# Performance work log

Measured on AMD Instinct MI355X. Metric: run time of the kernel, lower is better.

The kernel has to match this reference:

```python
import jax, jax.numpy as jnp
import numpy as np

T, IN, BATCH = 512, 512, 256
HID, WID = 1024, 512


def setup_inputs() -> dict:
    key = jax.random.key(0)
    k_x, k_wh, k_bh, k_wy, k_by, k_h0 = jax.random.split(key, 6)
    s_h = 1.0 / np.sqrt(HID + IN)  # stabilise sigmoid pre-activations
    s_y = 1.0 / np.sqrt(HID)
    return {
        "xs": jax.random.normal(k_x, (T, IN, BATCH), dtype=jnp.float32),
        "W_h": jax.random.normal(k_wh, (HID, HID + IN), dtype=jnp.float32) * s_h,
        "b_h": jax.random.normal(k_bh, (HID, 1), dtype=jnp.float32) * 0.1,
        "W_y": jax.random.normal(k_wy, (WID, HID), dtype=jnp.float32) * s_y,
        "b_y": jax.random.normal(k_by, (WID, 1), dtype=jnp.float32) * 0.1,
        "h0": jax.random.normal(k_h0, (HID, 1), dtype=jnp.float32),
    }


def reference(xs, W_h, b_h, W_y, b_y, h0):
    # xs: [T, input_size, batch]; returns ys: [T, width, batch]
    batch = xs.shape[2]
    h_init = jnp.tile(h0, (1, batch))  # [HID, batch]

    def step(h, x):
        z = jnp.concatenate([h, x], axis=0)          # [HID+IN, batch]
        h_new = jax.nn.sigmoid(W_h @ z + b_h)        # [HID, batch]
        y = jax.nn.sigmoid(W_y @ h_new + b_y)        # [WID, batch]
        return h_new, y

    _, ys = jax.lax.scan(step, h_init, xs)
    return ys
```

## Files before the change

kernel.cpp:

```cpp
#include <hip/hip_runtime.h>
#include <hip/hip_bf16.h>

#define T_STEPS 512
#define INP     512
#define NB      256
#define HID     1024
#define WID     512
#define KZ      1536
#define ZSZ     (NB * KZ)
#define ZR      6

typedef short          bf16x8   __attribute__((ext_vector_type(8)));
typedef float          f32x4    __attribute__((ext_vector_type(4)));
typedef float          f32x2    __attribute__((ext_vector_type(2)));
typedef unsigned short ushort8  __attribute__((ext_vector_type(8)));
typedef unsigned short ushort2v __attribute__((ext_vector_type(2)));
typedef unsigned short ushort4v __attribute__((ext_vector_type(4)));
typedef unsigned       uint4v   __attribute__((ext_vector_type(4)));
typedef unsigned long long u64;

__device__ __forceinline__ unsigned short f2bf(float x) {
  __hip_bfloat16 h = __float2bfloat16(x);
  return __builtin_bit_cast(unsigned short, h);
}
__device__ __forceinline__ float sigm(float x) { return 1.0f / (1.0f + __expf(-x)); }

#define ZLOAD_FAST(dst, p) \
  asm volatile("global_load_dwordx4 %0, %1, off sc0" : "=v"(dst) : "v"(p))
#define ZLOAD_SLOW(dst, p) \
  asm volatile("global_load_dwordx4 %0, %1, off sc0 sc1" : "=v"(dst) : "v"(p))
#define ZWAITN(n) do { \
  asm volatile("s_waitcnt vmcnt(" #n ")" ::: "memory"); \
  __builtin_amdgcn_sched_barrier(0); \
} while (0)

template <bool FAST>
__device__ __forceinline__ void zst4(unsigned short* p, ushort2v v) {
  if constexpr (FAST) *(unsigned*)p = __builtin_bit_cast(unsigned, v);
  else __hip_atomic_store((unsigned*)p, __builtin_bit_cast(unsigned, v),
                          __ATOMIC_RELAXED, __HIP_MEMORY_SCOPE_AGENT);
}
template <bool FAST>
__device__ __forceinline__ void zst8(unsigned short* p, ushort4v v) {
  if constexpr (FAST) *(u64*)p = __builtin_bit_cast(u64, v);
  else __hip_atomic_store((u64*)p, __builtin_bit_cast(u64, v),
                          __ATOMIC_RELAXED, __HIP_MEMORY_SCOPE_AGENT);
}

__device__ __forceinline__ void poll1(unsigned* p, unsigned tgt) {
  while (__hip_atomic_load(p, __ATOMIC_RELAXED, __HIP_MEMORY_SCOPE_AGENT) < tgt)
    __builtin_amdgcn_s_sleep(1);
}
__device__ __forceinline__ void pollh(unsigned* bar, unsigned ht, unsigned xt, unsigned yt) {
  uint4v v;
  for (;;) {
    asm volatile("global_load_dwordx4 %0, %1, off sc0 sc1\n\ts_waitcnt vmcnt(0)"
                 : "=v"(v) : "v"(bar) : "memory");
    if (v.x >= ht && v.y >= xt && v.z >= yt) return;
    __builtin_amdgcn_s_sleep(1);
  }
}
__device__ __forceinline__ void arrive(unsigned* ctr) {
  asm volatile("s_waitcnt vmcnt(0)" ::: "memory");
  __syncthreads();
  if (threadIdx.x == 0)
    __hip_atomic_fetch_add(ctr, 1u, __ATOMIC_RELAXED, __HIP_MEMORY_SCOPE_AGENT);
}

__global__ void elman_setup(const float* __restrict__ h0, const float* __restrict__ xs,
                            unsigned short* __restrict__ zT, unsigned* __restrict__ bars) {
  const int b = blockIdx.x;
  if (b == 0) {
    for (int j = threadIdx.x; j < 1024; j += blockDim.x) bars[j] = 0u;
  }
  for (int k = threadIdx.x; k < KZ; k += blockDim.x) {
    const float v = (k < HID) ? h0[k] : xs[(size_t)(k - HID) * NB + b];
    zT[(size_t)b * KZ + k] = f2bf(v);
  }
  for (int i = threadIdx.x; i < INP; i += blockDim.x) {
    zT[(size_t)ZSZ     + (size_t)b * KZ + HID + i] = f2bf(xs[(size_t)(INP     + i) * NB + b]);
    zT[(size_t)2 * ZSZ + (size_t)b * KZ + HID + i] = f2bf(xs[(size_t)(2 * INP + i) * NB + b]);
  }
}

#define PSTR 36
#define PWSZ (32 * PSTR)

template <bool FAST>
__device__ __forceinline__ void run_phases(
    const float* __restrict__ xs,
    const float* __restrict__ Wh, const float* __restrict__ bh,
    const float* __restrict__ Wy, const float* __restrict__ by,
    unsigned short* __restrict__ zT, float* __restrict__ out,
    unsigned* line, float* P, int wg, int tid) {
  const int w = tid >> 6, lane = tid & 63;
  const int lr = lane & 15, lk = lane >> 4;

  if (wg < 128) {
    const int m0 = (wg >> 3) * 64;
    const int n0 = (wg & 7) * 32;
    const int kw = w * 192;
    bf16x8 A[4][6];
#pragma unroll
    for (int mt = 0; mt < 4; ++mt)
#pragma unroll
      for (int kc = 0; kc < 6; ++kc) {
        const float* wp = Wh + (size_t)(m0 + mt * 16 + lr) * KZ + kw + kc * 32 + lk * 8;
        const f32x4 f0 = *(const f32x4*)wp;
        const f32x4 f1 = *(const f32x4*)(wp + 4);
        ushort8 a;
#pragma unroll
        for (int e = 0; e < 4; ++e) { a[e] = f2bf(f0[e]); a[4 + e] = f2bf(f1[e]); }
        A[mt][kc] = __builtin_bit_cast(bf16x8, a);
      }
    const int lcol = tid >> 4;
    const int r2 = (tid & 15) * 2;
    f32x2 bias[2];
#pragma unroll
    for (int hf = 0; hf < 2; ++hf) bias[hf] = *(const f32x2*)&bh[m0 + hf * 32 + r2];
    float* Pw = P + w * (2 * PWSZ);

    for (int t = 0; t <= T_STEPS; ++t) {
      if (t < T_STEPS) {
        const unsigned short* zc = zT + (size_t)(t % ZR) * ZSZ;
        unsigned short* zn = zT + (size_t)((t + 1) % ZR) * ZSZ;
        if (t >= 1) {
          if (tid == 0) pollh(line, 16u * (unsigned)t,
                              (t >= 3) ? 8u * (unsigned)(t - 2) : 0u,
                              (t >= 5) ? 8u * (unsigned)(t - 4) : 0u);
          __syncthreads();
        }
        const unsigned short* zb = zc + (size_t)(n0 + lr) * KZ + kw + lk * 8;
        bf16x8 bfr[6][2];
#pragma unroll
        for (int kc = 0; kc < 6; ++kc)
#pragma unroll
          for (int nt = 0; nt < 2; ++nt) {
            if constexpr (FAST) ZLOAD_FAST(bfr[kc][nt], zb + nt * (16 * KZ) + kc * 32);
            else                ZLOAD_SLOW(bfr[kc][nt], zb + nt * (16 * KZ) + kc * 32);
          }
        f32x4 acc[4][2];
#pragma unroll
        for (int mt = 0; mt < 4; ++mt)
#pragma unroll
          for (int nt = 0; nt < 2; ++nt) acc[mt][nt] = (f32x4){0.f, 0.f, 0.f, 0.f};
        ZWAITN(8);
#pragma unroll
        for (int kc = 0; kc < 2; ++kc)
#pragma unroll
          for (int nt = 0; nt < 2; ++nt)
#pragma unroll
            for (int mt = 0; mt < 4; ++mt)
              acc[mt][nt] = __builtin_amdgcn_mfma_f32_16x16x32_bf16(A[mt][kc], bfr[kc][nt], acc[mt][nt], 0, 0, 0);
        ZWAITN(4);
#pragma unroll
        for (int kc = 2; kc < 4; ++kc)
#pragma unroll
          for (int nt = 0; nt < 2; ++nt)
#pragma unroll
            for (int mt = 0; mt < 4; ++mt)
              acc[mt][nt] = __builtin_amdgcn_mfma_f32_16x16x32_bf16(A[mt][kc], bfr[kc][nt], acc[mt][nt], 0, 0, 0);
        ZWAITN(0);
#pragma unroll
        for (int kc = 4; kc < 6; ++kc)
#pragma unroll
          for (int nt = 0; nt < 2; ++nt)
#pragma unroll
            for (int mt = 0; mt < 4; ++mt)
              acc[mt][nt] = __builtin_amdgcn_mfma_f32_16x16x32_bf16(A[mt][kc], bfr[kc][nt], acc[mt][nt], 0, 0, 0);
#pragma unroll
        for (int hf = 0; hf < 2; ++hf)
#pragma unroll
          for (int mp = 0; mp < 2; ++mp)
#pragma unroll
            for (int nt = 0; nt < 2; ++nt)
              *(f32x4*)&Pw[hf * PWSZ + (nt * 16 + lr) * PSTR + mp * 16 + lk * 4] = acc[hf * 2 + mp][nt];
        __syncthreads();
#pragma unroll
        for (int hf = 0; hf < 2; ++hf) {
          f32x2 s = {0.f, 0.f};
#pragma unroll
          for (int ww = 0; ww < 8; ++ww)
            s += *(const f32x2*)&P[ww * (2 * PWSZ) + hf * PWSZ + lcol * PSTR + r2];
          s += bias[hf];
          ushort2v o2;
          o2[0] = f2bf(sigm(s[0]));
          o2[1] = f2bf(sigm(s[1]));
          zst4<FAST>(zn + (size_t)(n0 + lcol) * KZ + m0 + hf * 32 + r2, o2);
        }
      }
      arrive(line + 0);
    }

  } else if (wg < 192) {
    const int idx = wg - 128;
    const int m0 = (idx >> 3) * 64;
    const int n0 = (idx & 7) * 32;
    const int kw = w * 128;
    bf16x8 A[4][4];
#pragma unroll
    for (int mt = 0; mt < 4; ++mt)
#pragma unroll
      for (int kc = 0; kc < 4; ++kc) {
        const float* wp = Wy + (size_t)(m0 + mt * 16 + lr) * HID + kw + kc * 32 + lk * 8;
        const f32x4 f0 = *(const f32x4*)wp;
        const f32x4 f1 = *(const f32x4*)(wp + 4);
        ushort8 a;
#pragma unroll
        for (int e = 0; e < 4; ++e) { a[e] = f2bf(f0[e]); a[4 + e] = f2bf(f1[e]); }
        A[mt][kc] = __builtin_bit_cast(bf16x8, a);
      }
    const int lcol = tid & 31;
    const int r2 = (tid >> 5) * 2;
    f32x2 bias[2];
#pragma unroll
    for (int hf = 0; hf < 2; ++hf) bias[hf] = *(const f32x2*)&by[m0 + hf * 32 + r2];
    float* Pw = P + w * (2 * PWSZ);

    for (int t = 0; t <= T_STEPS; ++t) {
      if (t >= 1) {
        const unsigned short* zc = zT + (size_t)(t % ZR) * ZSZ;
        if (tid == 0) poll1(line + 0, 16u * (unsigned)t);
        __syncthreads();
        const unsigned short* zb = zc + (size_t)(n0 + lr) * KZ + kw + lk * 8;
        bf16x8 fb[4][2];
#pragma unroll
        for (int kc = 0; kc < 4; ++kc)
#pragma unroll
          for (int nt = 0; nt < 2; ++nt) {
            if constexpr (FAST) ZLOAD_FAST(fb[kc][nt], zb + nt * (16 * KZ) + kc * 32);
            else                ZLOAD_SLOW(fb[kc][nt], zb + nt * (16 * KZ) + kc * 32);
          }
        f32x4 acc[4][2];
#pragma unroll
        for (int mt = 0; mt < 4; ++mt)
#pragma unroll
          for (int nt = 0; nt < 2; ++nt) acc[mt][nt] = (f32x4){0.f, 0.f, 0.f, 0.f};
        ZWAITN(4);
#pragma unroll
        for (int kc = 0; kc < 2; ++kc)
#pragma unroll
          for (int nt = 0; nt < 2; ++nt)
#pragma unroll
            for (int mt = 0; mt < 4; ++mt)
              acc[mt][nt] = __builtin_amdgcn_mfma_f32_16x16x32_bf16(A[mt][kc], fb[kc][nt], acc[mt][nt], 0, 0, 0);
        ZWAITN(0);
#pragma unroll
        for (int kc = 2; kc < 4; ++kc)
#pragma unroll
          for (int nt = 0; nt < 2; ++nt)
#pragma unroll
            for (int mt = 0; mt < 4; ++mt)
              acc[mt][nt] = __builtin_amdgcn_mfma_f32_16x16x32_bf16(A[mt][kc], fb[kc][nt], acc[mt][nt], 0, 0, 0);
        float* op = out + (size_t)(t - 1) * (WID * NB);
#pragma unroll
        for (int hf = 0; hf < 2; ++hf)
#pragma unroll
          for (int mp = 0; mp < 2; ++mp)
#pragma unroll
            for (int nt = 0; nt < 2; ++nt)
              *(f32x4*)&Pw[hf * PWSZ + (nt * 16 + lr) * PSTR + mp * 16 + lk * 4] = acc[hf * 2 + mp][nt];
        __syncthreads();
#pragma unroll
        for (int hf = 0; hf < 2; ++hf) {
          f32x2 s = {0.f, 0.f};
#pragma unroll
          for (int ww = 0; ww < 8; ++ww)
            s += *(const f32x2*)&P[ww * (2 * PWSZ) + hf * PWSZ + lcol * PSTR + r2];
          s += bias[hf];
          const int row = m0 + hf * 32 + r2;
          op[(size_t)(row + 0) * NB + n0 + lcol] = sigm(s[0]);
          op[(size_t)(row + 1) * NB + n0 + lcol] = sigm(s[1]);
        }
      }
      arrive(line + 2);
    }

  } else {
    const int xi = wg - 192;
    const int i0 = (xi >> 3) * 64;
    const int b0 = (xi & 7) * 32;
    const int c = tid & 31, rb = tid >> 5;
    for (int t = 0; t <= T_STEPS; ++t) {
      if (t <= T_STEPS - 4) {
        unsigned short* zx = zT + (size_t)((t + 3) % ZR) * ZSZ;
        const float* xp = xs + (size_t)(t + 3) * (INP * NB) + (size_t)(i0 + rb * 4) * NB + b0 + c;
        ushort4v o;
#pragma unroll
        for (int j = 0; j < 4; ++j) o[j] = f2bf(xp[(size_t)j * NB]);
        if (t >= 3 && tid == 0) poll1(line + 0, 16u * (unsigned)(t - 2));
        __syncthreads();
        zst8<FAST>(zx + (size_t)(b0 + c) * KZ + HID + i0 + rb * 4, o);
      }
      arrive(line + 1);
    }
  }
}

__global__ void __launch_bounds__(512, 2) elman_seq(
    const float* __restrict__ xs,
    const float* __restrict__ Wh, const float* __restrict__ bh,
    const float* __restrict__ Wy, const float* __restrict__ by,
    unsigned short* __restrict__ zT, float* __restrict__ out,
    unsigned* __restrict__ bars) {
  __shared__ float P[16 * PWSZ];
  __shared__ unsigned modeSh;
  const int wg = blockIdx.x, tid = threadIdx.x;
  unsigned* line = bars + (wg & 7) * 64;
  unsigned* xcds = bars + 512;
  unsigned* hbar = bars + 768;

  unsigned xcc;
  asm volatile("s_getreg_b32 %0, hwreg(HW_REG_XCC_ID)" : "=s"(xcc));
  if (tid == 0) {
    __hip_atomic_store(&xcds[wg], xcc + 1u, __ATOMIC_RELAXED, __HIP_MEMORY_SCOPE_AGENT);
    asm volatile("s_waitcnt vmcnt(0)" ::: "memory");
    __hip_atomic_fetch_add(hbar, 1u, __ATOMIC_RELAXED, __HIP_MEMORY_SCOPE_AGENT);
    while (__hip_atomic_load(hbar, __ATOMIC_RELAXED, __HIP_MEMORY_SCOPE_AGENT) < 256u)
      __builtin_amdgcn_s_sleep(1);
    const unsigned v0 = __hip_atomic_load(&xcds[wg & 7], __ATOMIC_RELAXED, __HIP_MEMORY_SCOPE_AGENT);
    unsigned m = 1u;
    for (int j = 1; j < 32; ++j)
      m &= (__hip_atomic_load(&xcds[(wg & 7) + 8 * j], __ATOMIC_RELAXED,
                              __HIP_MEMORY_SCOPE_AGENT) == v0) ? 1u : 0u;
    modeSh = m;
  }
  __syncthreads();

  if (modeSh)
    run_phases<true >(xs, Wh, bh, Wy, by, zT, out, line, P, wg, tid);
  else
    run_phases<false>(xs, Wh, bh, Wy, by, zT, out, line, P, wg, tid);
}

extern "C" void kernel_launch(void* const* d_in, const int* in_sizes, int n_in,
                              void* d_out, int out_size, void* d_ws, size_t ws_size,
                              hipStream_t stream) {
  (void)in_sizes; (void)n_in; (void)out_size; (void)ws_size;
  const float* xs  = (const float*)d_in[0];
  const float* W_h = (const float*)d_in[1];
  const float* b_h = (const float*)d_in[2];
  const float* W_y = (const float*)d_in[3];
  const float* b_y = (const float*)d_in[4];
  const float* h0  = (const float*)d_in[5];
  float* out = (float*)d_out;

  unsigned short* zT = (unsigned short*)d_ws;
  unsigned* bars = (unsigned*)(zT + (size_t)ZR * ZSZ);

  elman_setup<<<dim3(NB), dim3(256), 0, stream>>>(h0, xs, zT, bars);

  void* args[8];
  args[0] = (void*)&xs;  args[1] = (void*)&W_h; args[2] = (void*)&b_h;
  args[3] = (void*)&W_y; args[4] = (void*)&b_y; args[5] = (void*)&zT;
  args[6] = (void*)&out; args[7] = (void*)&bars;
  hipLaunchCooperativeKernel((void*)elman_seq, dim3(256), dim3(512), args, 0u, stream);
}
```

Baseline: 2.608 ms.

## Compute x-part of hidden GEMM before waiting on the h barrier; mirror counter

```diff
diff --git a/kernel.cpp b/kernel.cpp
--- a/kernel.cpp
+++ b/kernel.cpp
@@ -65,6 +65,14 @@
   __syncthreads();
   if (threadIdx.x == 0)
     __hip_atomic_fetch_add(ctr, 1u, __ATOMIC_RELAXED, __HIP_MEMORY_SCOPE_AGENT);
+}
+__device__ __forceinline__ void arrive2(unsigned* ctr, unsigned* mir) {
+  asm volatile("s_waitcnt vmcnt(0)" ::: "memory");
+  __syncthreads();
+  if (threadIdx.x == 0) {
+    __hip_atomic_fetch_add(ctr, 1u, __ATOMIC_RELAXED, __HIP_MEMORY_SCOPE_AGENT);
+    __hip_atomic_fetch_add(mir, 1u, __ATOMIC_RELAXED, __HIP_MEMORY_SCOPE_AGENT);
+  }
 }
 
 __global__ void elman_setup(const float* __restrict__ h0, const float* __restrict__ xs,
@@ -99,13 +107,15 @@
   if (wg < 128) {
     const int m0 = (wg >> 3) * 64;
     const int n0 = (wg & 7) * 32;
-    const int kw = w * 192;
+    const int kwh = w * 128;
+    const int kwx = HID + w * 64;
     bf16x8 A[4][6];
 #pragma unroll
     for (int mt = 0; mt < 4; ++mt)
 #pragma unroll
       for (int kc = 0; kc < 6; ++kc) {
-        const float* wp = Wh + (size_t)(m0 + mt * 16 + lr) * KZ + kw + kc * 32 + lk * 8;
+        const int kg = (kc < 4) ? (kwh + kc * 32) : (kwx + (kc - 4) * 32);
+        const float* wp = Wh + (size_t)(m0 + mt * 16 + lr) * KZ + kg + lk * 8;
         const f32x4 f0 = *(const f32x4*)wp;
         const f32x4 f1 = *(const f32x4*)(wp + 4);
         ushort8 a;
@@ -124,50 +134,60 @@
       if (t < T_STEPS) {
         const unsigned short* zc = zT + (size_t)(t % ZR) * ZSZ;
         unsigned short* zn = zT + (size_t)((t + 1) % ZR) * ZSZ;
+        const unsigned short* zrow = zc + (size_t)(n0 + lr) * KZ;
+        const unsigned short* zbh = zrow + kwh + lk * 8;
+        const unsigned short* zbx = zrow + kwx + lk * 8;
+        bf16x8 fx[2][2];
+#pragma unroll
+        for (int j = 0; j < 2; ++j)
+#pragma unroll
+          for (int nt = 0; nt < 2; ++nt) {
+            if constexpr (FAST) ZLOAD_FAST(fx[j][nt], zbx + nt * (16 * KZ) + j * 32);
+            else                ZLOAD_SLOW(fx[j][nt], zbx + nt * (16 * KZ) + j * 32);
+          }
+        f32x4 acc[4][2];
+#pragma unroll
+        for (int mt = 0; mt < 4; ++mt)
+#pragma unroll
+          for (int nt = 0; nt < 2; ++nt) acc[mt][nt] = (f32x4){0.f, 0.f, 0.f, 0.f};
+        ZWAITN(0);
+#pragma unroll
+        for (int j = 0; j < 2; ++j)
+#pragma unroll
+          for (int nt = 0; nt < 2; ++nt)
+#pragma unroll
+            for (int mt = 0; mt < 4; ++mt)
+              acc[mt][nt] = __builtin_amdgcn_mfma_f32_16x16x32_bf16(A[mt][4 + j], fx[j][nt], acc[mt][nt], 0, 0, 0);
         if (t >= 1) {
           if (tid == 0) pollh(line, 16u * (unsigned)t,
-                              (t >= 3) ? 8u * (unsigned)(t - 2) : 0u,
+                              (t >= 2) ? 8u * (unsigned)(t - 1) : 0u,
                               (t >= 5) ? 8u * (unsigned)(t - 4) : 0u);
           __syncthreads();
         }
-        const unsigned short* zb = zc + (size_t)(n0 + lr) * KZ + kw + lk * 8;
-        bf16x8 bfr[6][2];
-#pragma unroll
-        for (int kc = 0; kc < 6; ++kc)
+        bf16x8 fh[4][2];
+#pragma unroll
+        for (int kc = 0; kc < 4; ++kc)
 #pragma unroll
           for (int nt = 0; nt < 2; ++nt) {
-            if constexpr (FAST) ZLOAD_FAST(bfr[kc][nt], zb + nt * (16 * KZ) + kc * 32);
-            else                ZLOAD_SLOW(bfr[kc][nt], zb + nt * (16 * KZ) + kc * 32);
+            if constexpr (FAST) ZLOAD_FAST(fh[kc][nt], zbh + nt * (16 * KZ) + kc * 32);
+            else                ZLOAD_SLOW(fh[kc][nt], zbh + nt * (16 * KZ) + kc * 32);
           }
-        f32x4 acc[4][2];
-#pragma unroll
-        for (int mt = 0; mt < 4; ++mt)
-#pragma unroll
-          for (int nt = 0; nt < 2; ++nt) acc[mt][nt] = (f32x4){0.f, 0.f, 0.f, 0.f};
-        ZWAITN(8);
+        ZWAITN(4);
 #pragma unroll
         for (int kc = 0; kc < 2; ++kc)
 #pragma unroll
           for (int nt = 0; nt < 2; ++nt)
 #pragma unroll
             for (int mt = 0; mt < 4; ++mt)
-              acc[mt][nt] = __builtin_amdgcn_mfma_f32_16x16x32_bf16(A[mt][kc], bfr[kc][nt], acc[mt][nt], 0, 0, 0);
-        ZWAITN(4);
+              acc[mt][nt] = __builtin_amdgcn_mfma_f32_16x16x32_bf16(A[mt][kc], fh[kc][nt], acc[mt][nt], 0, 0, 0);
+        ZWAITN(0);
 #pragma unroll
         for (int kc = 2; kc < 4; ++kc)
 #pragma unroll
           for (int nt = 0; nt < 2; ++nt)
 #pragma unroll
             for (int mt = 0; mt < 4; ++mt)
-              acc[mt][nt] = __builtin_amdgcn_mfma_f32_16x16x32_bf16(A[mt][kc], bfr[kc][nt], acc[mt][nt], 0, 0, 0);
-        ZWAITN(0);
-#pragma unroll
-        for (int kc = 4; kc < 6; ++kc)
-#pragma unroll
-          for (int nt = 0; nt < 2; ++nt)
-#pragma unroll
-            for (int mt = 0; mt < 4; ++mt)
-              acc[mt][nt] = __builtin_amdgcn_mfma_f32_16x16x32_bf16(A[mt][kc], bfr[kc][nt], acc[mt][nt], 0, 0, 0);
+              acc[mt][nt] = __builtin_amdgcn_mfma_f32_16x16x32_bf16(A[mt][kc], fh[kc][nt], acc[mt][nt], 0, 0, 0);
 #pragma unroll
         for (int hf = 0; hf < 2; ++hf)
 #pragma unroll
@@ -189,7 +209,7 @@
           zst4<FAST>(zn + (size_t)(n0 + lcol) * KZ + m0 + hf * 32 + r2, o2);
         }
       }
-      arrive(line + 0);
+      arrive2(line + 0, line + 32);
     }
 
   } else if (wg < 192) {
@@ -220,7 +240,7 @@
     for (int t = 0; t <= T_STEPS; ++t) {
       if (t >= 1) {
         const unsigned short* zc = zT + (size_t)(t % ZR) * ZSZ;
-        if (tid == 0) poll1(line + 0, 16u * (unsigned)t);
+        if (tid == 0) poll1(line + 32, 16u * (unsigned)t);
         __syncthreads();
         const unsigned short* zb = zc + (size_t)(n0 + lr) * KZ + kw + lk * 8;
         bf16x8 fb[4][2];
@@ -288,7 +308,7 @@
         ushort4v o;
 #pragma unroll
         for (int j = 0; j < 4; ++j) o[j] = f2bf(xp[(size_t)j * NB]);
-        if (t >= 3 && tid == 0) poll1(line + 0, 16u * (unsigned)(t - 2));
+        if (t >= 3 && tid == 0) poll1(line + 32, 16u * (unsigned)(t - 2));
         __syncthreads();
         zst8<FAST>(zx + (size_t)(b0 + c) * KZ + HID + i0 + rb * 4, o);
       }
```

New measurement: 2.851 ms. +9.3%, slower.
